# Performance work log

Hardware: AMD Instinct MI355X
Metric: run time of the kernel (lower is better)

The kernel has to match this reference:

```python
import jax, jax.numpy as jnp
import numpy as np

B, S, D = 4, 2048, 1024
H = 16
HD = D // H  # head_dim = 64

def setup_inputs() -> dict:
    key = jax.random.key(0)
    kx, kq, ko = jax.random.split(key, 3)
    # xavier-uniform-like scale for weights
    lim_qkv = (6.0 / (D + 3 * D)) ** 0.5
    lim_o = (6.0 / (D + D)) ** 0.5
    return {
        "x": jax.random.normal(kx, (B, S, D), dtype=jnp.float32),
        "w_qkv": jax.random.uniform(kq, (3 * D, D), jnp.float32, -lim_qkv, lim_qkv),
        "b_qkv": jnp.zeros((3 * D,), jnp.float32),
        "w_o": jax.random.uniform(ko, (D, D), jnp.float32, -lim_o, lim_o),
        "b_o": jnp.zeros((D,), jnp.float32),
    }

def reference(x, w_qkv, b_qkv, w_o, b_o):
    b, s, _ = x.shape
    # QKV projection: torch Linear computes x @ W^T + b
    qkv = jnp.einsum("bsd,ed->bse", x, w_qkv) + b_qkv          # [B,S,3D]
    qkv = qkv.reshape(b, s, H, 3 * HD).transpose(0, 2, 1, 3)    # [B,H,S,3*hd]
    q, k, v = jnp.split(qkv, 3, axis=-1)                        # each [B,H,S,hd]
    scale = 1.0 / jnp.sqrt(jnp.asarray(HD, dtype=q.dtype))
    logits = jnp.einsum("bhqd,bhkd->bhqk", q, k) * scale        # [B,H,S,S]
    attn = jax.nn.softmax(logits, axis=-1)
    vals = jnp.einsum("bhqk,bhkd->bhqd", attn, v)               # [B,H,S,hd]
    vals = vals.transpose(0, 2, 1, 3).reshape(b, s, H * HD)     # [B,S,D]
    return jnp.einsum("bsd,ed->bse", vals, w_o) + b_o
```

## Files before the change

kernel.cpp:

```cpp
#include <hip/hip_runtime.h>
#include <hip/hip_bf16.h>


typedef __attribute__((ext_vector_type(4))) float f32x4;
typedef __attribute__((ext_vector_type(8))) short s16x8;
typedef __attribute__((ext_vector_type(2))) unsigned u32x2;
typedef __attribute__((ext_vector_type(4))) unsigned u32x4;

constexpr size_t PART_ELEMS = (size_t)8192 * 1024;

__device__ __forceinline__ unsigned short f2bf(float f) {
  __hip_bfloat16 h = __float2bfloat16(f);
  unsigned short u;
  __builtin_memcpy(&u, &h, 2);
  return u;
}
__device__ __forceinline__ unsigned pack2bf(float a, float b) {
  return (unsigned)f2bf(a) | ((unsigned)f2bf(b) << 16);
}
__device__ __forceinline__ float fexp2(float x) {
#if __has_builtin(__builtin_amdgcn_exp2f)
  return __builtin_amdgcn_exp2f(x);
#else
  float r; asm("v_exp_f32 %0, %1" : "=v"(r) : "v"(x)); return r;
#endif
}
__device__ __forceinline__ void gload_lds16(const void* g, void* l) {
  __builtin_amdgcn_global_load_lds(
      (const __attribute__((address_space(1))) unsigned*)g,
      (__attribute__((address_space(3))) unsigned*)l, 16, 0, 0);
}
__device__ __forceinline__ int swzs(int row, int col) {
  return row * 64 + (((col >> 3) ^ (row & 7)) << 3) + (col & 7);
}

__global__ __launch_bounds__(256) void cvt2_kernel(
    const float* __restrict__ a, unsigned short* __restrict__ oa,
    const float* __restrict__ b, unsigned short* __restrict__ ob) {
  const int bid = blockIdx.x;
  const float* in;
  unsigned short* out;
  size_t i;
  if (bid < 4096) {
    in = a; out = oa; i = ((size_t)bid * 256 + threadIdx.x) * 8;
  } else {
    in = b; out = ob; i = ((size_t)(bid - 4096) * 256 + threadIdx.x) * 8;
  }
  f32x4 v0 = *reinterpret_cast<const f32x4*>(in + i);
  f32x4 v1 = *reinterpret_cast<const f32x4*>(in + i + 4);
  u32x4 pk;
  pk.x = pack2bf(v0.x, v0.y); pk.y = pack2bf(v0.z, v0.w);
  pk.z = pack2bf(v1.x, v1.y); pk.w = pack2bf(v1.z, v1.w);
  *reinterpret_cast<u32x4*>(out + i) = pk;
}

__global__ __launch_bounds__(256) void cvt_kernel(const float* __restrict__ in,
                                                  unsigned short* __restrict__ out) {
  const size_t i = ((size_t)blockIdx.x * 256 + threadIdx.x) * 8;
  f32x4 v0 = *reinterpret_cast<const f32x4*>(in + i);
  f32x4 v1 = *reinterpret_cast<const f32x4*>(in + i + 4);
  u32x4 pk;
  pk.x = pack2bf(v0.x, v0.y); pk.y = pack2bf(v0.z, v0.w);
  pk.z = pack2bf(v1.x, v1.y); pk.w = pack2bf(v1.z, v1.w);
  *reinterpret_cast<u32x4*>(out + i) = pk;
}

template <bool SCATTER>
__global__ __launch_bounds__(256) void gemm_bb(
    const unsigned short* __restrict__ A, const unsigned short* __restrict__ Bw,
    const float* __restrict__ bias, void* __restrict__ Cptr,
    int M, int N, int K) {
  __shared__ short lds_a[128 * 64];
  __shared__ short lds_b[128 * 64];
  const int t = threadIdx.x;
  const int l = t & 63;
  const int w = t >> 6;
  const int id = blockIdx.x;
  const int xcd = id & 7;
  const int rr = id >> 3;
  const int bm = (xcd * 8 + (rr & 7)) * 128;
  const int bn = (rr >> 3) * 128;
  const int wr = (w >> 1) * 64;
  const int wc = (w & 1) * 64;
  const int lr = l & 15;
  const int lkh = l >> 4;

  f32x4 acc[4][4] = {};

  const int c8 = l >> 3;
  const int gcol = ((l & 7) ^ c8) * 8;

  for (int k0 = 0; k0 < K; k0 += 64) {
    const unsigned short* as = &A[(size_t)(bm + w * 32 + c8) * K + k0 + gcol];
    const unsigned short* bs = &Bw[(size_t)(bn + w * 32 + c8) * K + k0 + gcol];
#pragma unroll
    for (int c = 0; c < 4; ++c) {
      gload_lds16(as + (size_t)(c * 8) * K, &lds_a[(w * 32 + c * 8) * 64]);
      gload_lds16(bs + (size_t)(c * 8) * K, &lds_b[(w * 32 + c * 8) * 64]);
    }
    __syncthreads();

#pragma unroll
    for (int ki = 0; ki < 2; ++ki) {
      s16x8 af[4], bfr[4];
#pragma unroll
      for (int mt = 0; mt < 4; ++mt) {
        const int row = wr + mt * 16 + lr;
        af[mt] = *reinterpret_cast<const s16x8*>(
            &lds_a[row * 64 + ((((ki << 2) + lkh) ^ (lr & 7)) << 3)]);
      }
#pragma unroll
      for (int nt = 0; nt < 4; ++nt) {
        const int row = wc + nt * 16 + lr;
        bfr[nt] = *reinterpret_cast<const s16x8*>(
            &lds_b[row * 64 + ((((ki << 2) + lkh) ^ (lr & 7)) << 3)]);
      }
#pragma unroll
      for (int mt = 0; mt < 4; ++mt)
#pragma unroll
        for (int nt = 0; nt < 4; ++nt)
          acc[mt][nt] = __builtin_amdgcn_mfma_f32_16x16x32_bf16(af[mt], bfr[nt], acc[mt][nt], 0, 0, 0);
    }
    __syncthreads();
  }

  if (SCATTER) {
    unsigned short* W = (unsigned short*)Cptr;
    const int s0 = (bm & 2047) + wr + (l >> 4) * 4;
    const int batch = bm >> 11;
#pragma unroll
    for (int nt = 0; nt < 4; ++nt) {
      const int col = bn + wc + nt * 16 + lr;
      const int h = col / 192;
      const int rem = col - h * 192;
      const int part = rem >> 6;
      const int d = rem & 63;
      const size_t bh = (size_t)batch * 16 + h;
      const float bv = bias[col];
      unsigned short* base;
      int stride;
      float scale;
      if (part == 2) {
        base = W + 2 * PART_ELEMS + (bh * 64 + d) * 2048;
        stride = 1;
        scale = 1.0f;
      } else {
        base = W + (size_t)part * PART_ELEMS + bh * 2048 * 64 + d;
        stride = 64;
        scale = (part == 0) ? 0.1803368801f : 1.0f;
      }
      unsigned short* p = base + (size_t)s0 * stride;
#pragma unroll
      for (int mt = 0; mt < 4; ++mt) {
        unsigned short* pm = p + mt * 16 * stride;
#pragma unroll
        for (int r = 0; r < 4; ++r)
          pm[r * stride] = f2bf((acc[mt][nt][r] + bv) * scale);
      }
    }
  } else {
    float* C = (float*)Cptr;
#pragma unroll
    for (int mt = 0; mt < 4; ++mt) {
#pragma unroll
      for (int nt = 0; nt < 4; ++nt) {
        const int col = bn + wc + nt * 16 + lr;
        const float bv = bias[col];
#pragma unroll
        for (int r = 0; r < 4; ++r) {
          const int row = bm + wr + mt * 16 + (l >> 4) * 4 + r;
          C[(size_t)row * N + col] = acc[mt][nt][r] + bv;
        }
      }
    }
  }
}

__global__ __launch_bounds__(512, 4) void attn_kernel(
    const unsigned short* __restrict__ ws, unsigned short* __restrict__ vals) {
  __shared__ short k_lds[2][64 * 64];
  __shared__ short vt_lds[2][64 * 64];
  __shared__ short p_lds[256 * 64];
  const int t = threadIdx.x;
  const int l = t & 63;
  const int w = t >> 6;
  const int lr = l & 15;
  const int lkh = l >> 4;
  const int f = blockIdx.x;
  const int xcd = f & 7;
  const int j = f >> 3;
  const int bh = xcd * 8 + (j & 7);
  const int qt = j >> 3;
  const int b = bh >> 4;
  const int h = bh & 15;
  const unsigned short* Qh  = ws + (size_t)bh * (2048 * 64);
  const unsigned short* Kh  = ws + PART_ELEMS + (size_t)bh * (2048 * 64);
  const unsigned short* VTh = ws + 2 * PART_ELEMS + (size_t)bh * (64 * 2048);

  const int srow = t >> 3;
  const int scol = (t & 7) * 8;

  s16x8 qf[2][2];
  {
    const unsigned short* qb = Qh + ((size_t)qt * 256 + w * 32 + lr) * 64 + lkh * 8;
    qf[0][0] = *reinterpret_cast<const s16x8*>(qb);
    qf[0][1] = *reinterpret_cast<const s16x8*>(qb + 32);
    qf[1][0] = *reinterpret_cast<const s16x8*>(qb + 16 * 64);
    qf[1][1] = *reinterpret_cast<const s16x8*>(qb + 16 * 64 + 32);
  }
  {
    s16x8 k0 = *reinterpret_cast<const s16x8*>(Kh + (size_t)srow * 64 + scol);
    s16x8 v0 = *reinterpret_cast<const s16x8*>(VTh + (size_t)srow * 2048 + scol);
    *reinterpret_cast<s16x8*>(&k_lds[0][swzs(srow, scol)])  = k0;
    *reinterpret_cast<s16x8*>(&vt_lds[0][swzs(srow, scol)]) = v0;
  }
  __syncthreads();

  f32x4 o_acc[2][4] = {};
  float l_s[2] = {0.f, 0.f};

  for (int kt = 0; kt < 32; ++kt) {
    const int cur = kt & 1;
    const int nxt = cur ^ 1;
    const bool pre = (kt + 1) < 32;

    s16x8 kr, vr;
    if (pre) {
      kr = *reinterpret_cast<const s16x8*>(Kh + ((size_t)(kt + 1) * 64 + srow) * 64 + scol);
      vr = *reinterpret_cast<const s16x8*>(VTh + (size_t)srow * 2048 + (kt + 1) * 64 + scol);
    }

    f32x4 s_acc[2][4] = {};
    {
      s16x8 kf[4][2];
#pragma unroll
      for (int nt = 0; nt < 4; ++nt) {
        kf[nt][0] = *reinterpret_cast<const s16x8*>(&k_lds[cur][swzs(nt * 16 + lr, lkh * 8)]);
        kf[nt][1] = *reinterpret_cast<const s16x8*>(&k_lds[cur][swzs(nt * 16 + lr, 32 + lkh * 8)]);
      }
      __builtin_amdgcn_s_setprio(1);
#pragma unroll
      for (int qh = 0; qh < 2; ++qh)
#pragma unroll
        for (int nt = 0; nt < 4; ++nt) {
          s_acc[qh][nt] = __builtin_amdgcn_mfma_f32_16x16x32_bf16(kf[nt][0], qf[qh][0], s_acc[qh][nt], 0, 0, 0);
          s_acc[qh][nt] = __builtin_amdgcn_mfma_f32_16x16x32_bf16(kf[nt][1], qf[qh][1], s_acc[qh][nt], 0, 0, 0);
        }
      __builtin_amdgcn_s_setprio(0);
    }

#pragma unroll
    for (int qh = 0; qh < 2; ++qh) {
      float rs = 0.f;
#pragma unroll
      for (int nt = 0; nt < 4; ++nt) {
        float p0 = fexp2(s_acc[qh][nt][0]);
        float p1 = fexp2(s_acc[qh][nt][1]);
        float p2 = fexp2(s_acc[qh][nt][2]);
        float p3 = fexp2(s_acc[qh][nt][3]);
        rs += (p0 + p1) + (p2 + p3);
        u32x2 pk;
        pk.x = pack2bf(p0, p1);
        pk.y = pack2bf(p2, p3);
        *reinterpret_cast<u32x2*>(&p_lds[swzs(w * 32 + qh * 16 + lr, nt * 16 + 4 * lkh)]) = pk;
      }
      l_s[qh] += rs;
    }

    {
      s16x8 vf[4][2];
#pragma unroll
      for (int nt = 0; nt < 4; ++nt) {
        vf[nt][0] = *reinterpret_cast<const s16x8*>(&vt_lds[cur][swzs(nt * 16 + lr, lkh * 8)]);
        vf[nt][1] = *reinterpret_cast<const s16x8*>(&vt_lds[cur][swzs(nt * 16 + lr, 32 + lkh * 8)]);
      }
      __builtin_amdgcn_s_setprio(1);
#pragma unroll
      for (int qh = 0; qh < 2; ++qh) {
        s16x8 pf0 = *reinterpret_cast<const s16x8*>(&p_lds[swzs(w * 32 + qh * 16 + lr, lkh * 8)]);
        s16x8 pf1 = *reinterpret_cast<const s16x8*>(&p_lds[swzs(w * 32 + qh * 16 + lr, 32 + lkh * 8)]);
#pragma unroll
        for (int nt = 0; nt < 4; ++nt) {
          o_acc[qh][nt] = __builtin_amdgcn_mfma_f32_16x16x32_bf16(pf0, vf[nt][0], o_acc[qh][nt], 0, 0, 0);
          o_acc[qh][nt] = __builtin_amdgcn_mfma_f32_16x16x32_bf16(pf1, vf[nt][1], o_acc[qh][nt], 0, 0, 0);
        }
      }
      __builtin_amdgcn_s_setprio(0);
    }

    if (pre) {
      *reinterpret_cast<s16x8*>(&k_lds[nxt][swzs(srow, scol)])  = kr;
      *reinterpret_cast<s16x8*>(&vt_lds[nxt][swzs(srow, scol)]) = vr;
    }
    __syncthreads();
  }

#pragma unroll
  for (int qh = 0; qh < 2; ++qh) {
    l_s[qh] += __shfl_xor(l_s[qh], 16);
    l_s[qh] += __shfl_xor(l_s[qh], 32);
  }
#pragma unroll
  for (int qh = 0; qh < 2; ++qh) {
#pragma unroll
    for (int r = 0; r < 4; ++r) {
      const float lv = __shfl(l_s[qh], 4 * lkh + r);
      const float inv = 1.0f / lv;
      const size_t row = (size_t)b * 2048 + qt * 256 + w * 32 + qh * 16 + lkh * 4 + r;
#pragma unroll
      for (int nt = 0; nt < 4; ++nt) {
        vals[row * 1024 + h * 64 + nt * 16 + lr] = f2bf(o_acc[qh][nt][r] * inv);
      }
    }
  }
}

extern "C" void kernel_launch(void* const* d_in, const int* in_sizes, int n_in,
                              void* d_out, int out_size, void* d_ws, size_t ws_size,
                              hipStream_t stream) {
  const float* x     = (const float*)d_in[0];
  const float* w_qkv = (const float*)d_in[1];
  const float* b_qkv = (const float*)d_in[2];
  const float* w_o   = (const float*)d_in[3];
  const float* b_o   = (const float*)d_in[4];
  float* out = (float*)d_out;

  unsigned short* xb     = (unsigned short*)d_ws;
  unsigned short* planes = xb + PART_ELEMS;
  unsigned short* wqkv_b = (unsigned short*)d_out;
  unsigned short* wo_b   = planes;

  cvt2_kernel<<<5632, 256, 0, stream>>>(x, xb, w_qkv, wqkv_b);
  gemm_bb<true><<<1536, 256, 0, stream>>>(
      xb, wqkv_b, b_qkv, planes, 8192, 3072, 1024);
  attn_kernel<<<512, 512, 0, stream>>>(planes, xb);
  cvt_kernel<<<512, 256, 0, stream>>>(w_o, wo_b);
  gemm_bb<false><<<512, 256, 0, stream>>>(
      xb, wo_b, b_o, out, 8192, 1024, 1024);
}
```

Before: 193.7 us.

## Switch attention to 32x32x16 MFMA with register-resident P and direct-to-LDS loads

Rewrites the attention inner loop to use 32x32x16 bf16 MFMA tiles instead of 16x16x32. The probability tile is now passed from the QK^T accumulator layout to the PV operand layout through cross-lane shuffles rather than a round trip through shared memory, so the P LDS buffer goes away. K/V tiles are staged with a global-to-LDS load helper per wave instead of register loads followed by LDS stores. The aim is fewer LDS writes and reads per tile and lower LDS usage, at the cost of extra shuffle work and reliance on the gload_lds16 helper and the swizzle matching the new per-wave staging layout.

New measurement: 206.6 us. 1.07x slower.

```diff
diff --git a/kernel.cpp b/kernel.cpp
--- a/kernel.cpp
+++ b/kernel.cpp
@@ -3,7 +3,9 @@
 
 
 typedef __attribute__((ext_vector_type(4))) float f32x4;
+typedef __attribute__((ext_vector_type(16))) float f32x16;
 typedef __attribute__((ext_vector_type(8))) short s16x8;
+typedef __attribute__((ext_vector_type(4))) short s16x4;
 typedef __attribute__((ext_vector_type(2))) unsigned u32x2;
 typedef __attribute__((ext_vector_type(4))) unsigned u32x4;
 
@@ -178,14 +180,13 @@
 
 __global__ __launch_bounds__(512, 4) void attn_kernel(
     const unsigned short* __restrict__ ws, unsigned short* __restrict__ vals) {
-  __shared__ short k_lds[2][64 * 64];
-  __shared__ short vt_lds[2][64 * 64];
-  __shared__ short p_lds[256 * 64];
+  __shared__ short k_lds[2 * 64 * 64];
+  __shared__ short vt_lds[2 * 64 * 64];
   const int t = threadIdx.x;
   const int l = t & 63;
   const int w = t >> 6;
-  const int lr = l & 15;
-  const int lkh = l >> 4;
+  const int l31 = l & 31;
+  const int hi = l >> 5;
   const int f = blockIdx.x;
   const int xcd = f & 7;
   const int j = f >> 3;
@@ -197,120 +198,103 @@
   const unsigned short* Kh  = ws + PART_ELEMS + (size_t)bh * (2048 * 64);
   const unsigned short* VTh = ws + 2 * PART_ELEMS + (size_t)bh * (64 * 2048);
 
-  const int srow = t >> 3;
-  const int scol = (t & 7) * 8;
-
-  s16x8 qf[2][2];
+  const int sr = l >> 3;
+  const int gcu = (l & 7) ^ sr;
+  const unsigned short* Ks = Kh + (size_t)(w * 8 + sr) * 64 + gcu * 8;
+  const unsigned short* Vs = VTh + (size_t)(w * 8 + sr) * 2048 + gcu * 8;
+  short* kd = &k_lds[w * 512];
+  short* vd = &vt_lds[w * 512];
+
+  s16x8 qf[4];
   {
-    const unsigned short* qb = Qh + ((size_t)qt * 256 + w * 32 + lr) * 64 + lkh * 8;
-    qf[0][0] = *reinterpret_cast<const s16x8*>(qb);
-    qf[0][1] = *reinterpret_cast<const s16x8*>(qb + 32);
-    qf[1][0] = *reinterpret_cast<const s16x8*>(qb + 16 * 64);
-    qf[1][1] = *reinterpret_cast<const s16x8*>(qb + 16 * 64 + 32);
-  }
-  {
-    s16x8 k0 = *reinterpret_cast<const s16x8*>(Kh + (size_t)srow * 64 + scol);
-    s16x8 v0 = *reinterpret_cast<const s16x8*>(VTh + (size_t)srow * 2048 + scol);
-    *reinterpret_cast<s16x8*>(&k_lds[0][swzs(srow, scol)])  = k0;
-    *reinterpret_cast<s16x8*>(&vt_lds[0][swzs(srow, scol)]) = v0;
-  }
+    const unsigned short* qb = Qh + ((size_t)qt * 256 + w * 32 + l31) * 64 + hi * 8;
+#pragma unroll
+    for (int s = 0; s < 4; ++s)
+      qf[s] = *reinterpret_cast<const s16x8*>(qb + s * 16);
+  }
+
+  gload_lds16(Ks, kd);
+  gload_lds16(Vs, vd);
   __syncthreads();
 
-  f32x4 o_acc[2][4] = {};
-  float l_s[2] = {0.f, 0.f};
+  f32x16 o_acc[2] = {};
+  float l_s = 0.f;
 
   for (int kt = 0; kt < 32; ++kt) {
     const int cur = kt & 1;
-    const int nxt = cur ^ 1;
-    const bool pre = (kt + 1) < 32;
-
-    s16x8 kr, vr;
-    if (pre) {
-      kr = *reinterpret_cast<const s16x8*>(Kh + ((size_t)(kt + 1) * 64 + srow) * 64 + scol);
-      vr = *reinterpret_cast<const s16x8*>(VTh + (size_t)srow * 2048 + (kt + 1) * 64 + scol);
-    }
-
-    f32x4 s_acc[2][4] = {};
-    {
-      s16x8 kf[4][2];
-#pragma unroll
-      for (int nt = 0; nt < 4; ++nt) {
-        kf[nt][0] = *reinterpret_cast<const s16x8*>(&k_lds[cur][swzs(nt * 16 + lr, lkh * 8)]);
-        kf[nt][1] = *reinterpret_cast<const s16x8*>(&k_lds[cur][swzs(nt * 16 + lr, 32 + lkh * 8)]);
-      }
+    if (kt + 1 < 32) {
+      gload_lds16(Ks + (size_t)(kt + 1) * 4096, kd + (cur ^ 1) * 4096);
+      gload_lds16(Vs + (size_t)(kt + 1) * 64, vd + (cur ^ 1) * 4096);
+    }
+    const short* kb = &k_lds[cur * 4096];
+    const short* vb = &vt_lds[cur * 4096];
+
+    f32x16 s_acc[2] = {};
+#pragma unroll
+    for (int c = 0; c < 2; ++c) {
+      s16x8 kf[4];
+#pragma unroll
+      for (int s = 0; s < 4; ++s)
+        kf[s] = *reinterpret_cast<const s16x8*>(&kb[swzs(c * 32 + l31, s * 16 + hi * 8)]);
       __builtin_amdgcn_s_setprio(1);
 #pragma unroll
-      for (int qh = 0; qh < 2; ++qh)
-#pragma unroll
-        for (int nt = 0; nt < 4; ++nt) {
-          s_acc[qh][nt] = __builtin_amdgcn_mfma_f32_16x16x32_bf16(kf[nt][0], qf[qh][0], s_acc[qh][nt], 0, 0, 0);
-          s_acc[qh][nt] = __builtin_amdgcn_mfma_f32_16x16x32_bf16(kf[nt][1], qf[qh][1], s_acc[qh][nt], 0, 0, 0);
-        }
+      for (int s = 0; s < 4; ++s)
+        s_acc[c] = __builtin_amdgcn_mfma_f32_32x32x16_bf16(kf[s], qf[s], s_acc[c], 0, 0, 0);
       __builtin_amdgcn_s_setprio(0);
     }
 
-#pragma unroll
-    for (int qh = 0; qh < 2; ++qh) {
-      float rs = 0.f;
-#pragma unroll
-      for (int nt = 0; nt < 4; ++nt) {
-        float p0 = fexp2(s_acc[qh][nt][0]);
-        float p1 = fexp2(s_acc[qh][nt][1]);
-        float p2 = fexp2(s_acc[qh][nt][2]);
-        float p3 = fexp2(s_acc[qh][nt][3]);
-        rs += (p0 + p1) + (p2 + p3);
-        u32x2 pk;
-        pk.x = pack2bf(p0, p1);
-        pk.y = pack2bf(p2, p3);
-        *reinterpret_cast<u32x2*>(&p_lds[swzs(w * 32 + qh * 16 + lr, nt * 16 + 4 * lkh)]) = pk;
-      }
-      l_s[qh] += rs;
-    }
-
-    {
-      s16x8 vf[4][2];
-#pragma unroll
-      for (int nt = 0; nt < 4; ++nt) {
-        vf[nt][0] = *reinterpret_cast<const s16x8*>(&vt_lds[cur][swzs(nt * 16 + lr, lkh * 8)]);
-        vf[nt][1] = *reinterpret_cast<const s16x8*>(&vt_lds[cur][swzs(nt * 16 + lr, 32 + lkh * 8)]);
-      }
+    unsigned u[2][8];
+    float rs = 0.f;
+#pragma unroll
+    for (int c = 0; c < 2; ++c)
+#pragma unroll
+      for (int i = 0; i < 8; ++i) {
+        const float p0 = fexp2(s_acc[c][2 * i]);
+        const float p1 = fexp2(s_acc[c][2 * i + 1]);
+        rs += p0 + p1;
+        u[c][i] = pack2bf(p0, p1);
+      }
+    l_s += rs;
+
+#pragma unroll
+    for (int ks = 0; ks < 4; ++ks) {
+      const int c = ks >> 1;
+      const int g = (ks & 1) * 4;
+      const unsigned u0 = u[c][g + 0], u1 = u[c][g + 1];
+      const unsigned u2 = u[c][g + 2], u3 = u[c][g + 3];
+      const unsigned p0 = (unsigned)__shfl_xor((int)u0, 32);
+      const unsigned p1 = (unsigned)__shfl_xor((int)u1, 32);
+      const unsigned p2 = (unsigned)__shfl_xor((int)u2, 32);
+      const unsigned p3 = (unsigned)__shfl_xor((int)u3, 32);
+      u32x4 pw;
+      pw.x = hi ? p2 : u0;
+      pw.y = hi ? p3 : u1;
+      pw.z = hi ? u2 : p0;
+      pw.w = hi ? u3 : p1;
+      const s16x8 pf = __builtin_bit_cast(s16x8, pw);
+      s16x8 vf0 = *reinterpret_cast<const s16x8*>(&vb[swzs(l31, ks * 16 + hi * 8)]);
+      s16x8 vf1 = *reinterpret_cast<const s16x8*>(&vb[swzs(32 + l31, ks * 16 + hi * 8)]);
       __builtin_amdgcn_s_setprio(1);
-#pragma unroll
-      for (int qh = 0; qh < 2; ++qh) {
-        s16x8 pf0 = *reinterpret_cast<const s16x8*>(&p_lds[swzs(w * 32 + qh * 16 + lr, lkh * 8)]);
-        s16x8 pf1 = *reinterpret_cast<const s16x8*>(&p_lds[swzs(w * 32 + qh * 16 + lr, 32 + lkh * 8)]);
-#pragma unroll
-        for (int nt = 0; nt < 4; ++nt) {
-          o_acc[qh][nt] = __builtin_amdgcn_mfma_f32_16x16x32_bf16(pf0, vf[nt][0], o_acc[qh][nt], 0, 0, 0);
-          o_acc[qh][nt] = __builtin_amdgcn_mfma_f32_16x16x32_bf16(pf1, vf[nt][1], o_acc[qh][nt], 0, 0, 0);
-        }
-      }
+      o_acc[0] = __builtin_amdgcn_mfma_f32_32x32x16_bf16(vf0, pf, o_acc[0], 0, 0, 0);
+      o_acc[1] = __builtin_amdgcn_mfma_f32_32x32x16_bf16(vf1, pf, o_acc[1], 0, 0, 0);
       __builtin_amdgcn_s_setprio(0);
     }
-
-    if (pre) {
-      *reinterpret_cast<s16x8*>(&k_lds[nxt][swzs(srow, scol)])  = kr;
-      *reinterpret_cast<s16x8*>(&vt_lds[nxt][swzs(srow, scol)]) = vr;
-    }
     __syncthreads();
   }
 
-#pragma unroll
-  for (int qh = 0; qh < 2; ++qh) {
-    l_s[qh] += __shfl_xor(l_s[qh], 16);
-    l_s[qh] += __shfl_xor(l_s[qh], 32);
-  }
-#pragma unroll
-  for (int qh = 0; qh < 2; ++qh) {
-#pragma unroll
-    for (int r = 0; r < 4; ++r) {
-      const float lv = __shfl(l_s[qh], 4 * lkh + r);
-      const float inv = 1.0f / lv;
-      const size_t row = (size_t)b * 2048 + qt * 256 + w * 32 + qh * 16 + lkh * 4 + r;
-#pragma unroll
-      for (int nt = 0; nt < 4; ++nt) {
-        vals[row * 1024 + h * 64 + nt * 16 + lr] = f2bf(o_acc[qh][nt][r] * inv);
-      }
+  l_s += __shfl_xor(l_s, 32);
+  const float inv = 1.0f / l_s;
+  const size_t row = (size_t)b * 2048 + qt * 256 + w * 32 + l31;
+  unsigned short* vout = vals + row * 1024 + h * 64 + 4 * hi;
+#pragma unroll
+  for (int db = 0; db < 2; ++db) {
+#pragma unroll
+    for (int g = 0; g < 4; ++g) {
+      s16x4 o4;
+#pragma unroll
+      for (int r = 0; r < 4; ++r)
+        o4[r] = (short)f2bf(o_acc[db][4 * g + r] * inv);
+      *reinterpret_cast<s16x4*>(&vout[db * 32 + 8 * g]) = o4;
     }
   }
 }
```

## Give each attention wave 64 query rows and stream K/V straight into LDS

Applied to the files above, without the earlier changes.

The attention kernel moves from 8 waves of 32 query rows to 4 waves of 64 query rows per block. Each K and V fragment read from LDS now feeds twice as many MFMAs. K and V^T tiles are also prefetched with direct global-to-LDS loads using a pre-swizzled source column, replacing the register-staged loads and LDS stores. The cost is more accumulator registers per wave and half as many threads per block, which lowers the wave count available to hide latency. Correctness depends on the source swizzle matching the swzs layout.

After: 202.6 us. +4.6%, slower.

```diff
diff --git a/kernel.cpp b/kernel.cpp
--- a/kernel.cpp
+++ b/kernel.cpp
@@ -176,7 +176,7 @@
   }
 }
 
-__global__ __launch_bounds__(512, 4) void attn_kernel(
+__global__ __launch_bounds__(256, 2) void attn_kernel(
     const unsigned short* __restrict__ ws, unsigned short* __restrict__ vals) {
   __shared__ short k_lds[2][64 * 64];
   __shared__ short vt_lds[2][64 * 64];
@@ -197,116 +197,111 @@
   const unsigned short* Kh  = ws + PART_ELEMS + (size_t)bh * (2048 * 64);
   const unsigned short* VTh = ws + 2 * PART_ELEMS + (size_t)bh * (64 * 2048);
 
-  const int srow = t >> 3;
-  const int scol = (t & 7) * 8;
-
-  s16x8 qf[2][2];
-  {
-    const unsigned short* qb = Qh + ((size_t)qt * 256 + w * 32 + lr) * 64 + lkh * 8;
-    qf[0][0] = *reinterpret_cast<const s16x8*>(qb);
-    qf[0][1] = *reinterpret_cast<const s16x8*>(qb + 32);
-    qf[1][0] = *reinterpret_cast<const s16x8*>(qb + 16 * 64);
-    qf[1][1] = *reinterpret_cast<const s16x8*>(qb + 16 * 64 + 32);
-  }
-  {
-    s16x8 k0 = *reinterpret_cast<const s16x8*>(Kh + (size_t)srow * 64 + scol);
-    s16x8 v0 = *reinterpret_cast<const s16x8*>(VTh + (size_t)srow * 2048 + scol);
-    *reinterpret_cast<s16x8*>(&k_lds[0][swzs(srow, scol)])  = k0;
-    *reinterpret_cast<s16x8*>(&vt_lds[0][swzs(srow, scol)]) = v0;
-  }
+  const int sr8 = l >> 3;
+  const int gcu = (l & 7) ^ sr8;
+  const unsigned short* Ks = Kh + (size_t)(w * 16 + sr8) * 64 + gcu * 8;
+  const unsigned short* Vs = VTh + (size_t)(w * 16 + sr8) * 2048 + gcu * 8;
+
+  s16x8 qf[4][2];
+#pragma unroll
+  for (int qh = 0; qh < 4; ++qh) {
+    const unsigned short* qb =
+        Qh + ((size_t)qt * 256 + w * 64 + qh * 16 + lr) * 64 + lkh * 8;
+    qf[qh][0] = *reinterpret_cast<const s16x8*>(qb);
+    qf[qh][1] = *reinterpret_cast<const s16x8*>(qb + 32);
+  }
+
+  gload_lds16(Ks, &k_lds[0][(w * 16) * 64]);
+  gload_lds16(Ks + 8 * 64, &k_lds[0][(w * 16 + 8) * 64]);
+  gload_lds16(Vs, &vt_lds[0][(w * 16) * 64]);
+  gload_lds16(Vs + 8 * 2048, &vt_lds[0][(w * 16 + 8) * 64]);
   __syncthreads();
 
-  f32x4 o_acc[2][4] = {};
-  float l_s[2] = {0.f, 0.f};
+  f32x4 o_acc[4][4] = {};
+  float l_s[4] = {0.f, 0.f, 0.f, 0.f};
 
   for (int kt = 0; kt < 32; ++kt) {
     const int cur = kt & 1;
     const int nxt = cur ^ 1;
-    const bool pre = (kt + 1) < 32;
-
-    s16x8 kr, vr;
-    if (pre) {
-      kr = *reinterpret_cast<const s16x8*>(Kh + ((size_t)(kt + 1) * 64 + srow) * 64 + scol);
-      vr = *reinterpret_cast<const s16x8*>(VTh + (size_t)srow * 2048 + (kt + 1) * 64 + scol);
-    }
-
-    f32x4 s_acc[2][4] = {};
-    {
-      s16x8 kf[4][2];
-#pragma unroll
-      for (int nt = 0; nt < 4; ++nt) {
-        kf[nt][0] = *reinterpret_cast<const s16x8*>(&k_lds[cur][swzs(nt * 16 + lr, lkh * 8)]);
-        kf[nt][1] = *reinterpret_cast<const s16x8*>(&k_lds[cur][swzs(nt * 16 + lr, 32 + lkh * 8)]);
-      }
+
+    if (kt + 1 < 32) {
+      const unsigned short* kp = Ks + (size_t)(kt + 1) * 4096;
+      const unsigned short* vp = Vs + (size_t)(kt + 1) * 64;
+      gload_lds16(kp, &k_lds[nxt][(w * 16) * 64]);
+      gload_lds16(kp + 8 * 64, &k_lds[nxt][(w * 16 + 8) * 64]);
+      gload_lds16(vp, &vt_lds[nxt][(w * 16) * 64]);
+      gload_lds16(vp + 8 * 2048, &vt_lds[nxt][(w * 16 + 8) * 64]);
+    }
+
+    s16x8 kf[4][2];
+#pragma unroll
+    for (int nt = 0; nt < 4; ++nt) {
+      kf[nt][0] = *reinterpret_cast<const s16x8*>(&k_lds[cur][swzs(nt * 16 + lr, lkh * 8)]);
+      kf[nt][1] = *reinterpret_cast<const s16x8*>(&k_lds[cur][swzs(nt * 16 + lr, 32 + lkh * 8)]);
+    }
+#pragma unroll
+    for (int qh = 0; qh < 4; ++qh) {
+      f32x4 s_acc[4] = {};
       __builtin_amdgcn_s_setprio(1);
 #pragma unroll
-      for (int qh = 0; qh < 2; ++qh)
-#pragma unroll
-        for (int nt = 0; nt < 4; ++nt) {
-          s_acc[qh][nt] = __builtin_amdgcn_mfma_f32_16x16x32_bf16(kf[nt][0], qf[qh][0], s_acc[qh][nt], 0, 0, 0);
-          s_acc[qh][nt] = __builtin_amdgcn_mfma_f32_16x16x32_bf16(kf[nt][1], qf[qh][1], s_acc[qh][nt], 0, 0, 0);
-        }
+      for (int nt = 0; nt < 4; ++nt) {
+        s_acc[nt] = __builtin_amdgcn_mfma_f32_16x16x32_bf16(kf[nt][0], qf[qh][0], s_acc[nt], 0, 0, 0);
+        s_acc[nt] = __builtin_amdgcn_mfma_f32_16x16x32_bf16(kf[nt][1], qf[qh][1], s_acc[nt], 0, 0, 0);
+      }
       __builtin_amdgcn_s_setprio(0);
-    }
-
-#pragma unroll
-    for (int qh = 0; qh < 2; ++qh) {
       float rs = 0.f;
 #pragma unroll
       for (int nt = 0; nt < 4; ++nt) {
-        float p0 = fexp2(s_acc[qh][nt][0]);
-        float p1 = fexp2(s_acc[qh][nt][1]);
-        float p2 = fexp2(s_acc[qh][nt][2]);
-        float p3 = fexp2(s_acc[qh][nt][3]);
+        float p0 = fexp2(s_acc[nt][0]);
+        float p1 = fexp2(s_acc[nt][1]);
+        float p2 = fexp2(s_acc[nt][2]);
+        float p3 = fexp2(s_acc[nt][3]);
         rs += (p0 + p1) + (p2 + p3);
         u32x2 pk;
         pk.x = pack2bf(p0, p1);
         pk.y = pack2bf(p2, p3);
-        *reinterpret_cast<u32x2*>(&p_lds[swzs(w * 32 + qh * 16 + lr, nt * 16 + 4 * lkh)]) = pk;
+        *reinterpret_cast<u32x2*>(
+            &p_lds[swzs(w * 64 + qh * 16 + lr, nt * 16 + 4 * lkh)]) = pk;
       }
       l_s[qh] += rs;
     }
 
-    {
-      s16x8 vf[4][2];
-#pragma unroll
-      for (int nt = 0; nt < 4; ++nt) {
-        vf[nt][0] = *reinterpret_cast<const s16x8*>(&vt_lds[cur][swzs(nt * 16 + lr, lkh * 8)]);
-        vf[nt][1] = *reinterpret_cast<const s16x8*>(&vt_lds[cur][swzs(nt * 16 + lr, 32 + lkh * 8)]);
-      }
+    s16x8 vf[4][2];
+#pragma unroll
+    for (int nt = 0; nt < 4; ++nt) {
+      vf[nt][0] = *reinterpret_cast<const s16x8*>(&vt_lds[cur][swzs(nt * 16 + lr, lkh * 8)]);
+      vf[nt][1] = *reinterpret_cast<const s16x8*>(&vt_lds[cur][swzs(nt * 16 + lr, 32 + lkh * 8)]);
+    }
+#pragma unroll
+    for (int qh = 0; qh < 4; ++qh) {
+      s16x8 pf0 = *reinterpret_cast<const s16x8*>(
+          &p_lds[swzs(w * 64 + qh * 16 + lr, lkh * 8)]);
+      s16x8 pf1 = *reinterpret_cast<const s16x8*>(
+          &p_lds[swzs(w * 64 + qh * 16 + lr, 32 + lkh * 8)]);
       __builtin_amdgcn_s_setprio(1);
 #pragma unroll
-      for (int qh = 0; qh < 2; ++qh) {
-        s16x8 pf0 = *reinterpret_cast<const s16x8*>(&p_lds[swzs(w * 32 + qh * 16 + lr, lkh * 8)]);
-        s16x8 pf1 = *reinterpret_cast<const s16x8*>(&p_lds[swzs(w * 32 + qh * 16 + lr, 32 + lkh * 8)]);
-#pragma unroll
-        for (int nt = 0; nt < 4; ++nt) {
-          o_acc[qh][nt] = __builtin_amdgcn_mfma_f32_16x16x32_bf16(pf0, vf[nt][0], o_acc[qh][nt], 0, 0, 0);
-          o_acc[qh][nt] = __builtin_amdgcn_mfma_f32_16x16x32_bf16(pf1, vf[nt][1], o_acc[qh][nt], 0, 0, 0);
-        }
+      for (int nt = 0; nt < 4; ++nt) {
+        o_acc[qh][nt] = __builtin_amdgcn_mfma_f32_16x16x32_bf16(pf0, vf[nt][0], o_acc[qh][nt], 0, 0, 0);
+        o_acc[qh][nt] = __builtin_amdgcn_mfma_f32_16x16x32_bf16(pf1, vf[nt][1], o_acc[qh][nt], 0, 0, 0);
       }
       __builtin_amdgcn_s_setprio(0);
     }
-
-    if (pre) {
-      *reinterpret_cast<s16x8*>(&k_lds[nxt][swzs(srow, scol)])  = kr;
-      *reinterpret_cast<s16x8*>(&vt_lds[nxt][swzs(srow, scol)]) = vr;
-    }
     __syncthreads();
   }
 
 #pragma unroll
-  for (int qh = 0; qh < 2; ++qh) {
+  for (int qh = 0; qh < 4; ++qh) {
     l_s[qh] += __shfl_xor(l_s[qh], 16);
     l_s[qh] += __shfl_xor(l_s[qh], 32);
   }
 #pragma unroll
-  for (int qh = 0; qh < 2; ++qh) {
+  for (int qh = 0; qh < 4; ++qh) {
 #pragma unroll
     for (int r = 0; r < 4; ++r) {
       const float lv = __shfl(l_s[qh], 4 * lkh + r);
       const float inv = 1.0f / lv;
-      const size_t row = (size_t)b * 2048 + qt * 256 + w * 32 + qh * 16 + lkh * 4 + r;
+      const size_t row =
+          (size_t)b * 2048 + qt * 256 + w * 64 + qh * 16 + lkh * 4 + r;
 #pragma unroll
       for (int nt = 0; nt < 4; ++nt) {
         vals[row * 1024 + h * 64 + nt * 16 + lr] = f2bf(o_acc[qh][nt][r] * inv);
@@ -333,7 +328,7 @@
   cvt2_kernel<<<5632, 256, 0, stream>>>(x, xb, w_qkv, wqkv_b);
   gemm_bb<true><<<1536, 256, 0, stream>>>(
       xb, wqkv_b, b_qkv, planes, 8192, 3072, 1024);
-  attn_kernel<<<512, 512, 0, stream>>>(planes, xb);
+  attn_kernel<<<512, 256, 0, stream>>>(planes, xb);
   cvt_kernel<<<512, 256, 0, stream>>>(w_o, wo_b);
   gemm_bb<false><<<512, 256, 0, stream>>>(
       xb, wo_b, b_o, out, 8192, 1024, 1024);
```
